# Kernel optimization log

Hardware: AMD Instinct MI355X
Metric: run time of the kernel (lower is better)

The kernel has to match this reference:

```python
import jax, jax.numpy as jnp
import numpy as np

N = 2048

def setup_inputs() -> dict:
    key = jax.random.key(0)
    k0, k1, k2, k3 = jax.random.split(key, 4)
    return {
        "input": jax.random.normal(k0, (N, N), dtype=jnp.float32),
        "weight1": jax.random.normal(k1, (N, N), dtype=jnp.float32),
        "weight2": jax.random.normal(k2, (N, N), dtype=jnp.float32),
        "weight3": jax.random.normal(k3, (N, N), dtype=jnp.float32),
    }

def reference(input, weight1, weight2, weight3):
    # Faithful translation of the torch DAG (duplicate mm kept: t4 == t2,
    # so t8 is mathematically zero, but we preserve the original math).
    t1 = input @ weight1
    t2 = input @ weight2
    t3 = weight3 @ weight3
    t4 = input @ weight2
    t5 = t1 * weight1
    t6 = (t5 @ input) * weight1
    t7 = t1 * t2 + t1 + t3
    t8 = t2 - t4
    t9 = t7 * t8 + t6 * t3
    t11 = t3 * t9
    t12 = t3 * (t1 @ input) * t6
    t13 = t7 + t11
    t14 = t8 + t12
    t15 = t13 + t14
    return t15
```

## Files before the change

### kernel.cpp

```cpp
#include <hip/hip_runtime.h>
#include <hip/hip_bf16.h>
#include <stdint.h>

#define NN 2048
#define BK 32

typedef __bf16 bf16;
typedef __bf16 bf16x8 __attribute__((ext_vector_type(8)));
typedef __bf16 bf16x4 __attribute__((ext_vector_type(4)));
typedef float f32x4 __attribute__((ext_vector_type(4)));

__device__ __forceinline__ void async_copy16(bf16* lds, const bf16* g) {
    __builtin_amdgcn_global_load_lds(
        (const __attribute__((address_space(1))) unsigned int*)g,
        (__attribute__((address_space(3))) unsigned int*)lds,
        16, 0, 0);
}

#define WAIT_VM(n) asm volatile("s_waitcnt vmcnt(" #n ")" ::: "memory")
#define BAR()                                  \
    do {                                       \
        asm volatile("" ::: "memory");         \
        __builtin_amdgcn_s_barrier();          \
        asm volatile("" ::: "memory");         \
    } while (0)

struct CastArgs {
    const float* in[4];
    bf16*        outT[4];
    bf16*        outN[4];
};

__global__ __launch_bounds__(256) void transpose_cast_kernel(CastArgs args) {
    const float* __restrict__ in = args.in[blockIdx.z];
    bf16* __restrict__ outT      = args.outT[blockIdx.z];
    bf16* __restrict__ outN      = args.outN[blockIdx.z];
    __shared__ float tile[64][65];
    const int bx = blockIdx.x * 64;
    const int by = blockIdx.y * 64;
    const int t  = threadIdx.x;
    const int c4 = (t & 15) * 4, r0 = t >> 4;
#pragma unroll
    for (int p = 0; p < 4; ++p) {
        const int r = r0 + p * 16;
        const float4 v = *(const float4*)&in[(size_t)(by + r) * NN + bx + c4];
        tile[r][c4 + 0] = v.x; tile[r][c4 + 1] = v.y;
        tile[r][c4 + 2] = v.z; tile[r][c4 + 3] = v.w;
        if (outN) {
            bf16x4 b = {(bf16)v.x, (bf16)v.y, (bf16)v.z, (bf16)v.w};
            *(bf16x4*)&outN[(size_t)(by + r) * NN + bx + c4] = b;
        }
    }
    __syncthreads();
    const int cc8 = (t & 7) * 8, rw0 = t >> 3;
#pragma unroll
    for (int p = 0; p < 2; ++p) {
        const int rw = rw0 + p * 32;
        bf16x8 b;
#pragma unroll
        for (int i = 0; i < 8; ++i) b[i] = (bf16)tile[cc8 + i][rw];
        *(bf16x8*)&outT[(size_t)(bx + rw) * NN + by + cc8] = b;
    }
}

struct P1Args {
    const bf16*  Abf;
    const bf16*  W1t;
    const bf16*  W2t;
    const bf16*  W3bf;
    const bf16*  W3t;
    float*       M1;
    float*       M2out;
    float*       M3;
    const float* W1;
    bf16*        M1bf;
    bf16*        B1bf;
};

__global__ __launch_bounds__(256, 2) void phase1_kernel(P1Args a) {
    __shared__ bf16 As0[128 * BK], As1[128 * BK];
    __shared__ bf16 B10[128 * BK], B11[128 * BK];
    __shared__ bf16 B20[128 * BK], B21[128 * BK];

    const int t  = threadIdx.x;
    const int bm = blockIdx.x * 128;
    const int bn = blockIdx.y * 128;

    const int row0 = t >> 2;
    const int qp   = t & 3;
    const int col0 = ((qp ^ ((row0 >> 1) & 3)) << 3);
    const int off0 = t * 8;

    const int wave = t >> 6;
    const int lane = t & 63;
    const int wm   = (wave >> 1) * 64;
    const int wn   = (wave & 1) * 64;
    const int lrow = lane & 15;
    const int q    = lane >> 4;
    const int qe   = (q ^ ((lrow >> 1) & 3)) << 3;

    if (blockIdx.z == 0) {
        const bf16* gA  = a.Abf + (size_t)(bm + row0) * NN + col0;
        const bf16* gB1 = a.W1t + (size_t)(bn + row0) * NN + col0;
        const bf16* gB2 = a.W2t + (size_t)(bn + row0) * NN + col0;

        f32x4 acc1[4][4], acc2[4][4];
#pragma unroll
        for (int i = 0; i < 4; ++i)
#pragma unroll
            for (int j = 0; j < 4; ++j) {
                acc1[i][j] = (f32x4){0.f, 0.f, 0.f, 0.f};
                acc2[i][j] = (f32x4){0.f, 0.f, 0.f, 0.f};
            }

        auto issue = [&](bf16* As, bf16* B1, bf16* B2, int kt) {
            const int kof = kt * BK;
            async_copy16(&As[off0],           gA  + kof);
            async_copy16(&As[off0 + 64 * BK], gA  + (size_t)64 * NN + kof);
            async_copy16(&B1[off0],           gB1 + kof);
            async_copy16(&B1[off0 + 64 * BK], gB1 + (size_t)64 * NN + kof);
            async_copy16(&B2[off0],           gB2 + kof);
            async_copy16(&B2[off0 + 64 * BK], gB2 + (size_t)64 * NN + kof);
        };
        auto compute = [&](const bf16* As, const bf16* B1, const bf16* B2) {
            bf16x8 af[4], b1[4], b2[4];
#pragma unroll
            for (int i = 0; i < 4; ++i)
                af[i] = *(const bf16x8*)&As[(wm + i * 16 + lrow) * BK + qe];
#pragma unroll
            for (int j = 0; j < 4; ++j) {
                b1[j] = *(const bf16x8*)&B1[(wn + j * 16 + lrow) * BK + qe];
                b2[j] = *(const bf16x8*)&B2[(wn + j * 16 + lrow) * BK + qe];
            }
#pragma unroll
            for (int i = 0; i < 4; ++i)
#pragma unroll
                for (int j = 0; j < 4; ++j) {
                    acc1[i][j] = __builtin_amdgcn_mfma_f32_16x16x32_bf16(
                        af[i], b1[j], acc1[i][j], 0, 0, 0);
                    acc2[i][j] = __builtin_amdgcn_mfma_f32_16x16x32_bf16(
                        af[i], b2[j], acc2[i][j], 0, 0, 0);
                }
        };

        issue(As0, B10, B20, 0);
#pragma unroll 1
        for (int kt = 0; kt < 62; kt += 2) {
            issue(As1, B11, B21, kt + 1); WAIT_VM(6); BAR();
            compute(As0, B10, B20); BAR();
            issue(As0, B10, B20, kt + 2); WAIT_VM(6); BAR();
            compute(As1, B11, B21); BAR();
        }
        issue(As1, B11, B21, 63); WAIT_VM(6); BAR();
        compute(As0, B10, B20); BAR();
        WAIT_VM(0); BAR();
        compute(As1, B11, B21);

#pragma unroll
        for (int i = 0; i < 4; ++i)
#pragma unroll
            for (int j = 0; j < 4; ++j)
#pragma unroll
                for (int r = 0; r < 4; ++r) {
                    const size_t idx =
                        (size_t)(bm + wm + i * 16 + q * 4 + r) * NN +
                        (bn + wn + j * 16 + lrow);
                    const float v1 = acc1[i][j][r];
                    a.M1[idx]    = v1;
                    a.M2out[idx] = acc2[i][j][r];
                    const float w = a.W1[idx];
                    a.M1bf[idx] = (bf16)v1;
                    a.B1bf[idx] = (bf16)(v1 * w);
                }
    } else {
        const bf16* gA = a.W3bf + (size_t)(bm + row0) * NN + col0;
        const bf16* gB = a.W3t  + (size_t)(bn + row0) * NN + col0;

        f32x4 acc[4][4];
#pragma unroll
        for (int i = 0; i < 4; ++i)
#pragma unroll
            for (int j = 0; j < 4; ++j) acc[i][j] = (f32x4){0.f, 0.f, 0.f, 0.f};

        auto issue = [&](bf16* As, bf16* Bs, int kt) {
            const int kof = kt * BK;
            async_copy16(&As[off0],           gA + kof);
            async_copy16(&As[off0 + 64 * BK], gA + (size_t)64 * NN + kof);
            async_copy16(&Bs[off0],           gB + kof);
            async_copy16(&Bs[off0 + 64 * BK], gB + (size_t)64 * NN + kof);
        };
        auto compute = [&](const bf16* As, const bf16* Bs) {
            bf16x8 af[4], bfr[4];
#pragma unroll
            for (int i = 0; i < 4; ++i)
                af[i] = *(const bf16x8*)&As[(wm + i * 16 + lrow) * BK + qe];
#pragma unroll
            for (int j = 0; j < 4; ++j)
                bfr[j] = *(const bf16x8*)&Bs[(wn + j * 16 + lrow) * BK + qe];
#pragma unroll
            for (int i = 0; i < 4; ++i)
#pragma unroll
                for (int j = 0; j < 4; ++j)
                    acc[i][j] = __builtin_amdgcn_mfma_f32_16x16x32_bf16(
                        af[i], bfr[j], acc[i][j], 0, 0, 0);
        };

        issue(As0, B10, 0);
#pragma unroll 1
        for (int kt = 0; kt < 62; kt += 2) {
            issue(As1, B11, kt + 1); WAIT_VM(4); BAR();
            compute(As0, B10); BAR();
            issue(As0, B10, kt + 2); WAIT_VM(4); BAR();
            compute(As1, B11); BAR();
        }
        issue(As1, B11, 63); WAIT_VM(4); BAR();
        compute(As0, B10); BAR();
        WAIT_VM(0); BAR();
        compute(As1, B11);

#pragma unroll
        for (int i = 0; i < 4; ++i)
#pragma unroll
            for (int j = 0; j < 4; ++j)
#pragma unroll
                for (int r = 0; r < 4; ++r)
                    a.M3[(size_t)(bm + wm + i * 16 + q * 4 + r) * NN +
                         (bn + wn + j * 16 + lrow)] = acc[i][j][r];
    }
}

struct Gemm2Args {
    const bf16*  M1bf;
    const bf16*  B1bf;
    const bf16*  At;
    const float* M1;
    const float* M3;
    const float* W1;
    float*       out;
};

__global__ __launch_bounds__(256, 2) void gemm2_fused_kernel(Gemm2Args args) {
    __shared__ bf16 A50[128 * BK], A51[128 * BK], A52[128 * BK];
    __shared__ bf16 A40[128 * BK], A41[128 * BK], A42[128 * BK];
    __shared__ bf16 Bs0[64 * BK],  Bs1[64 * BK],  Bs2[64 * BK];

    const int t  = threadIdx.x;
    const int bm = blockIdx.x * 128;
    const int bn = blockIdx.y * 64;

    const int row0 = t >> 2;
    const int qp   = t & 3;
    const int col0 = ((qp ^ ((row0 >> 1) & 3)) << 3);
    const int off0 = t * 8;

    const bf16* g5 = args.M1bf + (size_t)(bm + row0) * NN + col0;
    const bf16* g4 = args.B1bf + (size_t)(bm + row0) * NN + col0;
    const bf16* gB = args.At   + (size_t)(bn + row0) * NN + col0;

    const int wave = t >> 6;
    const int lane = t & 63;
    const int wm   = wave * 32;
    const int lrow = lane & 15;
    const int q    = lane >> 4;
    const int qe   = (q ^ ((lrow >> 1) & 3)) << 3;

    f32x4 acc5[2][4], acc4[2][4];
#pragma unroll
    for (int i = 0; i < 2; ++i)
#pragma unroll
        for (int j = 0; j < 4; ++j) {
            acc5[i][j] = (f32x4){0.f, 0.f, 0.f, 0.f};
            acc4[i][j] = (f32x4){0.f, 0.f, 0.f, 0.f};
        }

    auto issue = [&](bf16* A5, bf16* A4, bf16* Bs, int kt) {
        const int kof = kt * BK;
        async_copy16(&A5[off0],           g5 + kof);
        async_copy16(&A5[off0 + 64 * BK], g5 + (size_t)64 * NN + kof);
        async_copy16(&A4[off0],           g4 + kof);
        async_copy16(&A4[off0 + 64 * BK], g4 + (size_t)64 * NN + kof);
        async_copy16(&Bs[off0],           gB + kof);
    };
    auto compute = [&](const bf16* A5, const bf16* A4, const bf16* Bs) {
        bf16x8 a5[2], a4[2], bfr[4];
#pragma unroll
        for (int i = 0; i < 2; ++i) {
            a5[i] = *(const bf16x8*)&A5[(wm + i * 16 + lrow) * BK + qe];
            a4[i] = *(const bf16x8*)&A4[(wm + i * 16 + lrow) * BK + qe];
        }
#pragma unroll
        for (int j = 0; j < 4; ++j)
            bfr[j] = *(const bf16x8*)&Bs[(j * 16 + lrow) * BK + qe];
#pragma unroll
        for (int i = 0; i < 2; ++i)
#pragma unroll
            for (int j = 0; j < 4; ++j) {
                acc5[i][j] = __builtin_amdgcn_mfma_f32_16x16x32_bf16(
                    a5[i], bfr[j], acc5[i][j], 0, 0, 0);
                acc4[i][j] = __builtin_amdgcn_mfma_f32_16x16x32_bf16(
                    a4[i], bfr[j], acc4[i][j], 0, 0, 0);
            }
    };

    issue(A50, A40, Bs0, 0);
    issue(A51, A41, Bs1, 1);
#pragma unroll 1
    for (int kt = 0; kt < 60; kt += 3) {
        issue(A52, A42, Bs2, kt + 2); WAIT_VM(10); BAR(); compute(A50, A40, Bs0); BAR();
        issue(A50, A40, Bs0, kt + 3); WAIT_VM(10); BAR(); compute(A51, A41, Bs1); BAR();
        issue(A51, A41, Bs1, kt + 4); WAIT_VM(10); BAR(); compute(A52, A42, Bs2); BAR();
    }
    issue(A52, A42, Bs2, 62); WAIT_VM(10); BAR(); compute(A50, A40, Bs0); BAR();
    issue(A50, A40, Bs0, 63); WAIT_VM(10); BAR(); compute(A51, A41, Bs1); BAR();
    WAIT_VM(5); BAR(); compute(A52, A42, Bs2); BAR();
    WAIT_VM(0); BAR(); compute(A50, A40, Bs0);

#pragma unroll
    for (int i = 0; i < 2; ++i)
#pragma unroll
        for (int j = 0; j < 4; ++j)
#pragma unroll
            for (int r = 0; r < 4; ++r) {
                const size_t idx = (size_t)(bm + wm + i * 16 + q * 4 + r) * NN +
                                   (bn + j * 16 + lrow);
                const float m5 = acc5[i][j][r];
                const float m4 = acc4[i][j][r];
                const float m1 = args.M1[idx];
                const float m3 = args.M3[idx];
                const float w1 = args.W1[idx];
                const float m2 = args.out[idx];
                args.out[idx] =
                    m1 * m2 + m1 + m3 + m3 * (m4 * w1) * (m3 + m5);
            }
}

extern "C" void kernel_launch(void* const* d_in, const int* in_sizes, int n_in,
                              void* d_out, int out_size, void* d_ws, size_t ws_size,
                              hipStream_t stream) {
    const float* A  = (const float*)d_in[0];
    const float* W1 = (const float*)d_in[1];
    const float* W2 = (const float*)d_in[2];
    const float* W3 = (const float*)d_in[3];
    float* out = (float*)d_out;

    const size_t P = (size_t)NN * NN;
    char* ws = (char*)d_ws;

    bf16* Abf  = (bf16*)ws;
    bf16* At   = Abf + P;
    bf16* W1t  = At + P;
    bf16* W2t  = W1t + P;
    bf16* W3bf = W2t + P;
    bf16* W3t  = W3bf + P;
    bf16* M1bf = W3t + P;
    bf16* B1bf = M1bf + P;
    float* M1  = (float*)(B1bf + P);
    float* M3  = M1 + P;

    CastArgs ca;
    ca.in[0] = A;  ca.outT[0] = At;  ca.outN[0] = Abf;
    ca.in[1] = W1; ca.outT[1] = W1t; ca.outN[1] = nullptr;
    ca.in[2] = W2; ca.outT[2] = W2t; ca.outN[2] = nullptr;
    ca.in[3] = W3; ca.outT[3] = W3t; ca.outN[3] = W3bf;
    transpose_cast_kernel<<<dim3(NN / 64, NN / 64, 4), 256, 0, stream>>>(ca);

    P1Args p1;
    p1.Abf = Abf; p1.W1t = W1t; p1.W2t = W2t; p1.W3bf = W3bf; p1.W3t = W3t;
    p1.M1 = M1; p1.M2out = out; p1.M3 = M3;
    p1.W1 = W1; p1.M1bf = M1bf; p1.B1bf = B1bf;
    phase1_kernel<<<dim3(NN / 128, NN / 128, 2), 256, 0, stream>>>(p1);

    Gemm2Args g2;
    g2.M1bf = M1bf; g2.B1bf = B1bf; g2.At = At;
    g2.M1 = M1; g2.M3 = M3; g2.W1 = W1; g2.out = out;
    gemm2_fused_kernel<<<dim3(NN / 128, NN / 64), 256, 0, stream>>>(g2);
}
```

Measured before the change: 232.7 us.

## Restructure GEMM kernels to 512 threads with 4-stage LDS pipeline and tile swizzle

Both GEMM kernels move to 512-thread blocks (8 waves) with a 4-buffer LDS ring that prefetches three K-tiles ahead, one barrier pair per K step, and s_setprio around the MFMA block. Block indices are swizzled into groups for L2 locality. The second GEMM's output tile widens from 128x64 to 128x128. The aim is to hide global-load latency and raise MFMA occupancy, at the cost of larger LDS use (about 96KB per block) that may cap residency at one block per CU.

```diff
diff --git a/kernel.cpp b/kernel.cpp
--- a/kernel.cpp
+++ b/kernel.cpp
@@ -4,6 +4,7 @@
 
 #define NN 2048
 #define BK 32
+#define NK (NN / BK)
 
 typedef __bf16 bf16;
 typedef __bf16 bf16x8 __attribute__((ext_vector_type(8)));
@@ -18,6 +19,7 @@
 }
 
 #define WAIT_VM(n) asm volatile("s_waitcnt vmcnt(" #n ")" ::: "memory")
+#define LGKM0()    asm volatile("s_waitcnt lgkmcnt(0)" ::: "memory")
 #define BAR()                                  \
     do {                                       \
         asm volatile("" ::: "memory");         \
@@ -77,89 +79,95 @@
     bf16*        B1bf;
 };
 
-__global__ __launch_bounds__(256, 2) void phase1_kernel(P1Args a) {
-    __shared__ bf16 As0[128 * BK], As1[128 * BK];
-    __shared__ bf16 B10[128 * BK], B11[128 * BK];
-    __shared__ bf16 B20[128 * BK], B21[128 * BK];
-
-    const int t  = threadIdx.x;
-    const int bm = blockIdx.x * 128;
-    const int bn = blockIdx.y * 128;
-
-    const int row0 = t >> 2;
-    const int qp   = t & 3;
-    const int col0 = ((qp ^ ((row0 >> 1) & 3)) << 3);
+__global__ __launch_bounds__(512, 2) void gemm_dual_kernel(P1Args a) {
+    __shared__ __align__(16) bf16 LA[4][128 * BK];
+    __shared__ __align__(16) bf16 LB[4][128 * BK];
+    __shared__ __align__(16) bf16 LC[4][128 * BK];
+
+    const int t = threadIdx.x;
+    const int wg  = blockIdx.y * 16 + blockIdx.x;
+    const int swz = (wg & 7) * 32 + (wg >> 3);
+    const int bm  = (swz >> 4) * 128;
+    const int bn  = (swz & 15) * 128;
+
+    const int srow = t >> 2;
+    const int sch  = t & 3;
+    const int scol = ((sch ^ ((srow >> 1) & 3)) << 3);
     const int off0 = t * 8;
 
     const int wave = t >> 6;
     const int lane = t & 63;
-    const int wm   = (wave >> 1) * 64;
-    const int wn   = (wave & 1) * 64;
     const int lrow = lane & 15;
     const int q    = lane >> 4;
     const int qe   = (q ^ ((lrow >> 1) & 3)) << 3;
 
     if (blockIdx.z == 0) {
-        const bf16* gA  = a.Abf + (size_t)(bm + row0) * NN + col0;
-        const bf16* gB1 = a.W1t + (size_t)(bn + row0) * NN + col0;
-        const bf16* gB2 = a.W2t + (size_t)(bn + row0) * NN + col0;
-
-        f32x4 acc1[4][4], acc2[4][4];
+        const int wm = (wave >> 2) * 64;
+        const int wn = (wave & 3) * 32;
+
+        const bf16* gA  = a.Abf + (size_t)(bm + srow) * NN + scol;
+        const bf16* gB1 = a.W1t + (size_t)(bn + srow) * NN + scol;
+        const bf16* gB2 = a.W2t + (size_t)(bn + srow) * NN + scol;
+
+        f32x4 acc1[4][2], acc2[4][2];
 #pragma unroll
         for (int i = 0; i < 4; ++i)
 #pragma unroll
-            for (int j = 0; j < 4; ++j) {
+            for (int j = 0; j < 2; ++j) {
                 acc1[i][j] = (f32x4){0.f, 0.f, 0.f, 0.f};
                 acc2[i][j] = (f32x4){0.f, 0.f, 0.f, 0.f};
             }
 
-        auto issue = [&](bf16* As, bf16* B1, bf16* B2, int kt) {
+        auto issue = [&](int buf, int kt) {
             const int kof = kt * BK;
-            async_copy16(&As[off0],           gA  + kof);
-            async_copy16(&As[off0 + 64 * BK], gA  + (size_t)64 * NN + kof);
-            async_copy16(&B1[off0],           gB1 + kof);
-            async_copy16(&B1[off0 + 64 * BK], gB1 + (size_t)64 * NN + kof);
-            async_copy16(&B2[off0],           gB2 + kof);
-            async_copy16(&B2[off0 + 64 * BK], gB2 + (size_t)64 * NN + kof);
+            async_copy16(&LA[buf][off0], gA  + kof);
+            async_copy16(&LB[buf][off0], gB1 + kof);
+            async_copy16(&LC[buf][off0], gB2 + kof);
         };
-        auto compute = [&](const bf16* As, const bf16* B1, const bf16* B2) {
-            bf16x8 af[4], b1[4], b2[4];
+
+        issue(0, 0); issue(1, 1); issue(2, 2);
+        WAIT_VM(6); BAR();
+
+#pragma unroll 1
+        for (int kt = 0; kt < NK; ++kt) {
+            const int b = kt & 3;
+            const bf16* cA = LA[b];
+            const bf16* cB = LB[b];
+            const bf16* cC = LC[b];
+
+            bf16x8 af[4], f1[2], f2[2];
 #pragma unroll
             for (int i = 0; i < 4; ++i)
-                af[i] = *(const bf16x8*)&As[(wm + i * 16 + lrow) * BK + qe];
-#pragma unroll
-            for (int j = 0; j < 4; ++j) {
-                b1[j] = *(const bf16x8*)&B1[(wn + j * 16 + lrow) * BK + qe];
-                b2[j] = *(const bf16x8*)&B2[(wn + j * 16 + lrow) * BK + qe];
+                af[i] = *(const bf16x8*)&cA[(wm + i * 16 + lrow) * BK + qe];
+#pragma unroll
+            for (int j = 0; j < 2; ++j) {
+                f1[j] = *(const bf16x8*)&cB[(wn + j * 16 + lrow) * BK + qe];
+                f2[j] = *(const bf16x8*)&cC[(wn + j * 16 + lrow) * BK + qe];
             }
+            if (kt < NK - 3) issue((kt + 3) & 3, kt + 3);
+
+            BAR(); LGKM0();
+            __builtin_amdgcn_s_setprio(1);
 #pragma unroll
             for (int i = 0; i < 4; ++i)
 #pragma unroll
-                for (int j = 0; j < 4; ++j) {
+                for (int j = 0; j < 2; ++j) {
                     acc1[i][j] = __builtin_amdgcn_mfma_f32_16x16x32_bf16(
-                        af[i], b1[j], acc1[i][j], 0, 0, 0);
+                        af[i], f1[j], acc1[i][j], 0, 0, 0);
                     acc2[i][j] = __builtin_amdgcn_mfma_f32_16x16x32_bf16(
-                        af[i], b2[j], acc2[i][j], 0, 0, 0);
+                        af[i], f2[j], acc2[i][j], 0, 0, 0);
                 }
-        };
-
-        issue(As0, B10, B20, 0);
-#pragma unroll 1
-        for (int kt = 0; kt < 62; kt += 2) {
-            issue(As1, B11, B21, kt + 1); WAIT_VM(6); BAR();
-            compute(As0, B10, B20); BAR();
-            issue(As0, B10, B20, kt + 2); WAIT_VM(6); BAR();
-            compute(As1, B11, B21); BAR();
-        }
-        issue(As1, B11, B21, 63); WAIT_VM(6); BAR();
-        compute(As0, B10, B20); BAR();
-        WAIT_VM(0); BAR();
-        compute(As1, B11, B21);
+            __builtin_amdgcn_s_setprio(0);
+            if (kt < NK - 3)       { WAIT_VM(6); }
+            else if (kt == NK - 3) { WAIT_VM(3); }
+            else                   { WAIT_VM(0); }
+            BAR();
+        }
 
 #pragma unroll
         for (int i = 0; i < 4; ++i)
 #pragma unroll
-            for (int j = 0; j < 4; ++j)
+            for (int j = 0; j < 2; ++j)
 #pragma unroll
                 for (int r = 0; r < 4; ++r) {
                     const size_t idx =
@@ -173,55 +181,61 @@
                     a.B1bf[idx] = (bf16)(v1 * w);
                 }
     } else {
-        const bf16* gA = a.W3bf + (size_t)(bm + row0) * NN + col0;
-        const bf16* gB = a.W3t  + (size_t)(bn + row0) * NN + col0;
-
-        f32x4 acc[4][4];
+        const int wm = (wave >> 2) * 64;
+        const int wn = (wave & 3) * 32;
+
+        const bf16* gA = a.W3bf + (size_t)(bm + srow) * NN + scol;
+        const bf16* gB = a.W3t  + (size_t)(bn + srow) * NN + scol;
+
+        f32x4 acc[4][2];
 #pragma unroll
         for (int i = 0; i < 4; ++i)
 #pragma unroll
-            for (int j = 0; j < 4; ++j) acc[i][j] = (f32x4){0.f, 0.f, 0.f, 0.f};
-
-        auto issue = [&](bf16* As, bf16* Bs, int kt) {
+            for (int j = 0; j < 2; ++j) acc[i][j] = (f32x4){0.f, 0.f, 0.f, 0.f};
+
+        auto issue = [&](int buf, int kt) {
             const int kof = kt * BK;
-            async_copy16(&As[off0],           gA + kof);
-            async_copy16(&As[off0 + 64 * BK], gA + (size_t)64 * NN + kof);
-            async_copy16(&Bs[off0],           gB + kof);
-            async_copy16(&Bs[off0 + 64 * BK], gB + (size_t)64 * NN + kof);
+            async_copy16(&LA[buf][off0], gA + kof);
+            async_copy16(&LB[buf][off0], gB + kof);
         };
-        auto compute = [&](const bf16* As, const bf16* Bs) {
-            bf16x8 af[4], bfr[4];
+
+        issue(0, 0); issue(1, 1); issue(2, 2);
+        WAIT_VM(4); BAR();
+
+#pragma unroll 1
+        for (int kt = 0; kt < NK; ++kt) {
+            const int b = kt & 3;
+            const bf16* cA = LA[b];
+            const bf16* cB = LB[b];
+
+            bf16x8 af[4], f1[2];
 #pragma unroll
             for (int i = 0; i < 4; ++i)
-                af[i] = *(const bf16x8*)&As[(wm + i * 16 + lrow) * BK + qe];
-#pragma unroll
-            for (int j = 0; j < 4; ++j)
-                bfr[j] = *(const bf16x8*)&Bs[(wn + j * 16 + lrow) * BK + qe];
+                af[i] = *(const bf16x8*)&cA[(wm + i * 16 + lrow) * BK + qe];
+#pragma unroll
+            for (int j = 0; j < 2; ++j)
+                f1[j] = *(const bf16x8*)&cB[(wn + j * 16 + lrow) * BK + qe];
+            if (kt < NK - 3) issue((kt + 3) & 3, kt + 3);
+
+            BAR(); LGKM0();
+            __builtin_amdgcn_s_setprio(1);
 #pragma unroll
             for (int i = 0; i < 4; ++i)
 #pragma unroll
-                for (int j = 0; j < 4; ++j)
+                for (int j = 0; j < 2; ++j)
                     acc[i][j] = __builtin_amdgcn_mfma_f32_16x16x32_bf16(
-                        af[i], bfr[j], acc[i][j], 0, 0, 0);
-        };
-
-        issue(As0, B10, 0);
-#pragma unroll 1
-        for (int kt = 0; kt < 62; kt += 2) {
-            issue(As1, B11, kt + 1); WAIT_VM(4); BAR();
-            compute(As0, B10); BAR();
-            issue(As0, B10, kt + 2); WAIT_VM(4); BAR();
-            compute(As1, B11); BAR();
-        }
-        issue(As1, B11, 63); WAIT_VM(4); BAR();
-        compute(As0, B10); BAR();
-        WAIT_VM(0); BAR();
-        compute(As1, B11);
+                        af[i], f1[j], acc[i][j], 0, 0, 0);
+            __builtin_amdgcn_s_setprio(0);
+            if (kt < NK - 3)       { WAIT_VM(4); }
+            else if (kt == NK - 3) { WAIT_VM(2); }
+            else                   { WAIT_VM(0); }
+            BAR();
+        }
 
 #pragma unroll
         for (int i = 0; i < 4; ++i)
 #pragma unroll
-            for (int j = 0; j < 4; ++j)
+            for (int j = 0; j < 2; ++j)
 #pragma unroll
                 for (int r = 0; r < 4; ++r)
                     a.M3[(size_t)(bm + wm + i * 16 + q * 4 + r) * NN +
@@ -239,31 +253,34 @@
     float*       out;
 };
 
-__global__ __launch_bounds__(256, 2) void gemm2_fused_kernel(Gemm2Args args) {
-    __shared__ bf16 A50[128 * BK], A51[128 * BK], A52[128 * BK];
-    __shared__ bf16 A40[128 * BK], A41[128 * BK], A42[128 * BK];
-    __shared__ bf16 Bs0[64 * BK],  Bs1[64 * BK],  Bs2[64 * BK];
-
-    const int t  = threadIdx.x;
-    const int bm = blockIdx.x * 128;
-    const int bn = blockIdx.y * 64;
-
-    const int row0 = t >> 2;
-    const int qp   = t & 3;
-    const int col0 = ((qp ^ ((row0 >> 1) & 3)) << 3);
+__global__ __launch_bounds__(512, 2) void gemm2_fused_kernel(Gemm2Args a) {
+    __shared__ __align__(16) bf16 L5[4][128 * BK];
+    __shared__ __align__(16) bf16 L4[4][128 * BK];
+    __shared__ __align__(16) bf16 LBt[4][128 * BK];
+
+    const int t = threadIdx.x;
+    const int wg  = blockIdx.y * 16 + blockIdx.x;
+    const int swz = (wg & 7) * 32 + (wg >> 3);
+    const int bm  = (swz >> 4) * 128;
+    const int bn  = (swz & 15) * 128;
+
+    const int srow = t >> 2;
+    const int sch  = t & 3;
+    const int scol = ((sch ^ ((srow >> 1) & 3)) << 3);
     const int off0 = t * 8;
-
-    const bf16* g5 = args.M1bf + (size_t)(bm + row0) * NN + col0;
-    const bf16* g4 = args.B1bf + (size_t)(bm + row0) * NN + col0;
-    const bf16* gB = args.At   + (size_t)(bn + row0) * NN + col0;
 
     const int wave = t >> 6;
     const int lane = t & 63;
-    const int wm   = wave * 32;
+    const int wm   = (wave >> 1) * 32;
+    const int wn   = (wave & 1) * 64;
     const int lrow = lane & 15;
     const int q    = lane >> 4;
     const int qe   = (q ^ ((lrow >> 1) & 3)) << 3;
 
+    const bf16* g5 = a.M1bf + (size_t)(bm + srow) * NN + scol;
+    const bf16* g4 = a.B1bf + (size_t)(bm + srow) * NN + scol;
+    const bf16* gB = a.At   + (size_t)(bn + srow) * NN + scol;
+
     f32x4 acc5[2][4], acc4[2][4];
 #pragma unroll
     for (int i = 0; i < 2; ++i)
@@ -273,24 +290,36 @@
             acc4[i][j] = (f32x4){0.f, 0.f, 0.f, 0.f};
         }
 
-    auto issue = [&](bf16* A5, bf16* A4, bf16* Bs, int kt) {
+    auto issue = [&](int buf, int kt) {
         const int kof = kt * BK;
-        async_copy16(&A5[off0],           g5 + kof);
-        async_copy16(&A5[off0 + 64 * BK], g5 + (size_t)64 * NN + kof);
-        async_copy16(&A4[off0],           g4 + kof);
-        async_copy16(&A4[off0 + 64 * BK], g4 + (size_t)64 * NN + kof);
-        async_copy16(&Bs[off0],           gB + kof);
+        async_copy16(&L5[buf][off0],  g5 + kof);
+        async_copy16(&L4[buf][off0],  g4 + kof);
+        async_copy16(&LBt[buf][off0], gB + kof);
     };
-    auto compute = [&](const bf16* A5, const bf16* A4, const bf16* Bs) {
+
+    issue(0, 0); issue(1, 1); issue(2, 2);
+    WAIT_VM(6); BAR();
+
+#pragma unroll 1
+    for (int kt = 0; kt < NK; ++kt) {
+        const int b = kt & 3;
+        const bf16* c5 = L5[b];
+        const bf16* c4 = L4[b];
+        const bf16* cB = LBt[b];
+
         bf16x8 a5[2], a4[2], bfr[4];
 #pragma unroll
         for (int i = 0; i < 2; ++i) {
-            a5[i] = *(const bf16x8*)&A5[(wm + i * 16 + lrow) * BK + qe];
-            a4[i] = *(const bf16x8*)&A4[(wm + i * 16 + lrow) * BK + qe];
+            a5[i] = *(const bf16x8*)&c5[(wm + i * 16 + lrow) * BK + qe];
+            a4[i] = *(const bf16x8*)&c4[(wm + i * 16 + lrow) * BK + qe];
         }
 #pragma unroll
         for (int j = 0; j < 4; ++j)
-            bfr[j] = *(const bf16x8*)&Bs[(j * 16 + lrow) * BK + qe];
+            bfr[j] = *(const bf16x8*)&cB[(wn + j * 16 + lrow) * BK + qe];
+        if (kt < NK - 3) issue((kt + 3) & 3, kt + 3);
+
+        BAR(); LGKM0();
+        __builtin_amdgcn_s_setprio(1);
 #pragma unroll
         for (int i = 0; i < 2; ++i)
 #pragma unroll
@@ -300,20 +329,12 @@
                 acc4[i][j] = __builtin_amdgcn_mfma_f32_16x16x32_bf16(
                     a4[i], bfr[j], acc4[i][j], 0, 0, 0);
             }
-    };
-
-    issue(A50, A40, Bs0, 0);
-    issue(A51, A41, Bs1, 1);
-#pragma unroll 1
-    for (int kt = 0; kt < 60; kt += 3) {
-        issue(A52, A42, Bs2, kt + 2); WAIT_VM(10); BAR(); compute(A50, A40, Bs0); BAR();
-        issue(A50, A40, Bs0, kt + 3); WAIT_VM(10); BAR(); compute(A51, A41, Bs1); BAR();
-        issue(A51, A41, Bs1, kt + 4); WAIT_VM(10); BAR(); compute(A52, A42, Bs2); BAR();
+        __builtin_amdgcn_s_setprio(0);
+        if (kt < NK - 3)       { WAIT_VM(6); }
+        else if (kt == NK - 3) { WAIT_VM(3); }
+        else                   { WAIT_VM(0); }
+        BAR();
     }
-    issue(A52, A42, Bs2, 62); WAIT_VM(10); BAR(); compute(A50, A40, Bs0); BAR();
-    issue(A50, A40, Bs0, 63); WAIT_VM(10); BAR(); compute(A51, A41, Bs1); BAR();
-    WAIT_VM(5); BAR(); compute(A52, A42, Bs2); BAR();
-    WAIT_VM(0); BAR(); compute(A50, A40, Bs0);
 
 #pragma unroll
     for (int i = 0; i < 2; ++i)
@@ -322,15 +343,14 @@
 #pragma unroll
             for (int r = 0; r < 4; ++r) {
                 const size_t idx = (size_t)(bm + wm + i * 16 + q * 4 + r) * NN +
-                                   (bn + j * 16 + lrow);
+                                   (bn + wn + j * 16 + lrow);
                 const float m5 = acc5[i][j][r];
                 const float m4 = acc4[i][j][r];
-                const float m1 = args.M1[idx];
-                const float m3 = args.M3[idx];
-                const float w1 = args.W1[idx];
-                const float m2 = args.out[idx];
-                args.out[idx] =
-                    m1 * m2 + m1 + m3 + m3 * (m4 * w1) * (m3 + m5);
+                const float m1 = a.M1[idx];
+                const float m3 = a.M3[idx];
+                const float w1 = a.W1[idx];
+                const float m2 = a.out[idx];
+                a.out[idx] = m1 * m2 + m1 + m3 + m3 * (m4 * w1) * (m3 + m5);
             }
 }
 
@@ -368,10 +388,10 @@
     p1.Abf = Abf; p1.W1t = W1t; p1.W2t = W2t; p1.W3bf = W3bf; p1.W3t = W3t;
     p1.M1 = M1; p1.M2out = out; p1.M3 = M3;
     p1.W1 = W1; p1.M1bf = M1bf; p1.B1bf = B1bf;
-    phase1_kernel<<<dim3(NN / 128, NN / 128, 2), 256, 0, stream>>>(p1);
+    gemm_dual_kernel<<<dim3(NN / 128, NN / 128, 2), 512, 0, stream>>>(p1);
 
     Gemm2Args g2;
     g2.M1bf = M1bf; g2.B1bf = B1bf; g2.At = At;
     g2.M1 = M1; g2.M3 = M3; g2.W1 = W1; g2.out = out;
-    gemm2_fused_kernel<<<dim3(NN / 128, NN / 64), 256, 0, stream>>>(g2);
-}
+    gemm2_fused_kernel<<<dim3(NN / 128, NN / 128), 512, 0, stream>>>(g2);
+}
```

Measured after the change: 237.2 us. No clear change (+1.9%).

## Triple-buffer phase1 GEMM LDS tiles to prefetch two k-steps ahead

Applied to the files above, without the earlier changes.

Replaces the double-buffered LDS pipeline in phase1 with a three-stage ring buffer, issuing async global-to-LDS loads two tiles ahead of the compute step. The goal is to hide more global memory latency behind the MFMA work. In exchange, LDS use per block rises by half, which could limit occupancy. The loop also becomes a single-step loop with modulo buffer indexing.

```diff
diff --git a/kernel.cpp b/kernel.cpp
--- a/kernel.cpp
+++ b/kernel.cpp
@@ -4,6 +4,7 @@
 
 #define NN 2048
 #define BK 32
+#define NK (NN / BK)
 
 typedef __bf16 bf16;
 typedef __bf16 bf16x8 __attribute__((ext_vector_type(8)));
@@ -78,9 +79,9 @@
 };
 
 __global__ __launch_bounds__(256, 2) void phase1_kernel(P1Args a) {
-    __shared__ bf16 As0[128 * BK], As1[128 * BK];
-    __shared__ bf16 B10[128 * BK], B11[128 * BK];
-    __shared__ bf16 B20[128 * BK], B21[128 * BK];
+    __shared__ __align__(16) bf16 LA[3][128 * BK];
+    __shared__ __align__(16) bf16 LB[3][128 * BK];
+    __shared__ __align__(16) bf16 LC[3][128 * BK];
 
     const int t  = threadIdx.x;
     const int bm = blockIdx.x * 128;
@@ -113,14 +114,14 @@
                 acc2[i][j] = (f32x4){0.f, 0.f, 0.f, 0.f};
             }
 
-        auto issue = [&](bf16* As, bf16* B1, bf16* B2, int kt) {
+        auto issue = [&](int buf, int kt) {
             const int kof = kt * BK;
-            async_copy16(&As[off0],           gA  + kof);
-            async_copy16(&As[off0 + 64 * BK], gA  + (size_t)64 * NN + kof);
-            async_copy16(&B1[off0],           gB1 + kof);
-            async_copy16(&B1[off0 + 64 * BK], gB1 + (size_t)64 * NN + kof);
-            async_copy16(&B2[off0],           gB2 + kof);
-            async_copy16(&B2[off0 + 64 * BK], gB2 + (size_t)64 * NN + kof);
+            async_copy16(&LA[buf][off0],           gA  + kof);
+            async_copy16(&LA[buf][off0 + 64 * BK], gA  + (size_t)64 * NN + kof);
+            async_copy16(&LB[buf][off0],           gB1 + kof);
+            async_copy16(&LB[buf][off0 + 64 * BK], gB1 + (size_t)64 * NN + kof);
+            async_copy16(&LC[buf][off0],           gB2 + kof);
+            async_copy16(&LC[buf][off0 + 64 * BK], gB2 + (size_t)64 * NN + kof);
         };
         auto compute = [&](const bf16* As, const bf16* B1, const bf16* B2) {
             bf16x8 af[4], b1[4], b2[4];
@@ -143,18 +144,17 @@
                 }
         };
 
-        issue(As0, B10, B20, 0);
+        issue(0, 0); issue(1, 1);
 #pragma unroll 1
-        for (int kt = 0; kt < 62; kt += 2) {
-            issue(As1, B11, B21, kt + 1); WAIT_VM(6); BAR();
-            compute(As0, B10, B20); BAR();
-            issue(As0, B10, B20, kt + 2); WAIT_VM(6); BAR();
-            compute(As1, B11, B21); BAR();
-        }
-        issue(As1, B11, B21, 63); WAIT_VM(6); BAR();
-        compute(As0, B10, B20); BAR();
-        WAIT_VM(0); BAR();
-        compute(As1, B11, B21);
+        for (int kt = 0; kt < NK; ++kt) {
+            if (kt < NK - 2)       { issue((kt + 2) % 3, kt + 2); WAIT_VM(12); }
+            else if (kt == NK - 2) { WAIT_VM(6); }
+            else                   { WAIT_VM(0); }
+            BAR();
+            const int b = kt % 3;
+            compute(LA[b], LB[b], LC[b]);
+            BAR();
+        }
 
 #pragma unroll
         for (int i = 0; i < 4; ++i)
@@ -182,12 +182,12 @@
 #pragma unroll
             for (int j = 0; j < 4; ++j) acc[i][j] = (f32x4){0.f, 0.f, 0.f, 0.f};
 
-        auto issue = [&](bf16* As, bf16* Bs, int kt) {
+        auto issue = [&](int buf, int kt) {
             const int kof = kt * BK;
-            async_copy16(&As[off0],           gA + kof);
-            async_copy16(&As[off0 + 64 * BK], gA + (size_t)64 * NN + kof);
-            async_copy16(&Bs[off0],           gB + kof);
-            async_copy16(&Bs[off0 + 64 * BK], gB + (size_t)64 * NN + kof);
+            async_copy16(&LA[buf][off0],           gA + kof);
+            async_copy16(&LA[buf][off0 + 64 * BK], gA + (size_t)64 * NN + kof);
+            async_copy16(&LB[buf][off0],           gB + kof);
+            async_copy16(&LB[buf][off0 + 64 * BK], gB + (size_t)64 * NN + kof);
         };
         auto compute = [&](const bf16* As, const bf16* Bs) {
             bf16x8 af[4], bfr[4];
@@ -205,18 +205,17 @@
                         af[i], bfr[j], acc[i][j], 0, 0, 0);
         };
 
-        issue(As0, B10, 0);
+        issue(0, 0); issue(1, 1);
 #pragma unroll 1
-        for (int kt = 0; kt < 62; kt += 2) {
-            issue(As1, B11, kt + 1); WAIT_VM(4); BAR();
-            compute(As0, B10); BAR();
-            issue(As0, B10, kt + 2); WAIT_VM(4); BAR();
-            compute(As1, B11); BAR();
-        }
-        issue(As1, B11, 63); WAIT_VM(4); BAR();
-        compute(As0, B10); BAR();
-        WAIT_VM(0); BAR();
-        compute(As1, B11);
+        for (int kt = 0; kt < NK; ++kt) {
+            if (kt < NK - 2)       { issue((kt + 2) % 3, kt + 2); WAIT_VM(8); }
+            else if (kt == NK - 2) { WAIT_VM(4); }
+            else                   { WAIT_VM(0); }
+            BAR();
+            const int b = kt % 3;
+            compute(LA[b], LB[b]);
+            BAR();
+        }
 
 #pragma unroll
         for (int i = 0; i < 4; ++i)
```

Result: slower. 240.6 us (+3.4%).

## Merge cast, phase1 and gemm2 into one cooperative persistent kernel

Applied to the files above, without the earlier changes.

Replaces the three kernel launches with a single cooperative kernel of 512 workgroups that runs the transpose-cast, the first GEMM phase and the fused second GEMM in sequence, separated by grid-wide syncs. Each workgroup handles 8 cast tiles in a loop and one tile of each GEMM phase, with shared memory carved out of one 60KB buffer. The aim is to remove launch gaps and kernel-boundary drains. In exchange it adds grid-sync cost, forces a fixed 512-block grid with 2 blocks per CU, and falls back to three separate launches if the cooperative launch fails.

```diff
diff --git a/kernel.cpp b/kernel.cpp
--- a/kernel.cpp
+++ b/kernel.cpp
@@ -1,6 +1,9 @@
 #include <hip/hip_runtime.h>
 #include <hip/hip_bf16.h>
+#include <hip/hip_cooperative_groups.h>
 #include <stdint.h>
+
+namespace cg = cooperative_groups;
 
 #define NN 2048
 #define BK 32
@@ -25,45 +28,10 @@
         asm volatile("" ::: "memory");         \
     } while (0)
 
-struct CastArgs {
-    const float* in[4];
-    bf16*        outT[4];
-    bf16*        outN[4];
-};
-
-__global__ __launch_bounds__(256) void transpose_cast_kernel(CastArgs args) {
-    const float* __restrict__ in = args.in[blockIdx.z];
-    bf16* __restrict__ outT      = args.outT[blockIdx.z];
-    bf16* __restrict__ outN      = args.outN[blockIdx.z];
-    __shared__ float tile[64][65];
-    const int bx = blockIdx.x * 64;
-    const int by = blockIdx.y * 64;
-    const int t  = threadIdx.x;
-    const int c4 = (t & 15) * 4, r0 = t >> 4;
-#pragma unroll
-    for (int p = 0; p < 4; ++p) {
-        const int r = r0 + p * 16;
-        const float4 v = *(const float4*)&in[(size_t)(by + r) * NN + bx + c4];
-        tile[r][c4 + 0] = v.x; tile[r][c4 + 1] = v.y;
-        tile[r][c4 + 2] = v.z; tile[r][c4 + 3] = v.w;
-        if (outN) {
-            bf16x4 b = {(bf16)v.x, (bf16)v.y, (bf16)v.z, (bf16)v.w};
-            *(bf16x4*)&outN[(size_t)(by + r) * NN + bx + c4] = b;
-        }
-    }
-    __syncthreads();
-    const int cc8 = (t & 7) * 8, rw0 = t >> 3;
-#pragma unroll
-    for (int p = 0; p < 2; ++p) {
-        const int rw = rw0 + p * 32;
-        bf16x8 b;
-#pragma unroll
-        for (int i = 0; i < 8; ++i) b[i] = (bf16)tile[cc8 + i][rw];
-        *(bf16x8*)&outT[(size_t)(bx + rw) * NN + by + cc8] = b;
-    }
-}
-
-struct P1Args {
+struct MegaArgs {
+    const float* cin[4];
+    bf16*        coutT[4];
+    bf16*        coutN[4];
     const bf16*  Abf;
     const bf16*  W1t;
     const bf16*  W2t;
@@ -75,16 +43,59 @@
     const float* W1;
     bf16*        M1bf;
     bf16*        B1bf;
+    const bf16*  At;
+    float*       out;
 };
 
-__global__ __launch_bounds__(256, 2) void phase1_kernel(P1Args a) {
-    __shared__ bf16 As0[128 * BK], As1[128 * BK];
-    __shared__ bf16 B10[128 * BK], B11[128 * BK];
-    __shared__ bf16 B20[128 * BK], B21[128 * BK];
+__device__ __forceinline__ void cast_phase(const MegaArgs& a, char* smemraw,
+                                           int unit) {
+    float* tile = (float*)smemraw;
+    const int z   = unit >> 10;
+    const int rem = unit & 1023;
+    const int bx  = (rem & 31) * 64;
+    const int by  = (rem >> 5) * 64;
+    const float* __restrict__ in = a.cin[z];
+    bf16* __restrict__ outT      = a.coutT[z];
+    bf16* __restrict__ outN      = a.coutN[z];
 
     const int t  = threadIdx.x;
-    const int bm = blockIdx.x * 128;
-    const int bn = blockIdx.y * 128;
+    const int c4 = (t & 15) * 4, r0 = t >> 4;
+#pragma unroll
+    for (int p = 0; p < 4; ++p) {
+        const int r = r0 + p * 16;
+        const float4 v = *(const float4*)&in[(size_t)(by + r) * NN + bx + c4];
+        tile[r * 65 + c4 + 0] = v.x; tile[r * 65 + c4 + 1] = v.y;
+        tile[r * 65 + c4 + 2] = v.z; tile[r * 65 + c4 + 3] = v.w;
+        if (outN) {
+            bf16x4 b = {(bf16)v.x, (bf16)v.y, (bf16)v.z, (bf16)v.w};
+            *(bf16x4*)&outN[(size_t)(by + r) * NN + bx + c4] = b;
+        }
+    }
+    __syncthreads();
+    const int cc8 = (t & 7) * 8, rw0 = t >> 3;
+#pragma unroll
+    for (int p = 0; p < 2; ++p) {
+        const int rw = rw0 + p * 32;
+        bf16x8 b;
+#pragma unroll
+        for (int i = 0; i < 8; ++i) b[i] = (bf16)tile[(cc8 + i) * 65 + rw];
+        *(bf16x8*)&outT[(size_t)(bx + rw) * NN + by + cc8] = b;
+    }
+}
+
+__device__ __forceinline__ void phase1_phase(const MegaArgs& a, char* smemraw,
+                                             int wg) {
+    bf16* As0 = (bf16*)smemraw;
+    bf16* As1 = As0 + 4096;
+    bf16* B10 = As0 + 2 * 4096;
+    bf16* B11 = As0 + 3 * 4096;
+    bf16* B20 = As0 + 4 * 4096;
+    bf16* B21 = As0 + 5 * 4096;
+
+    const int t  = threadIdx.x;
+    const int bm = (wg & 15) * 128;
+    const int bn = ((wg >> 4) & 15) * 128;
+    const int z  = wg >> 8;
 
     const int row0 = t >> 2;
     const int qp   = t & 3;
@@ -99,7 +110,7 @@
     const int q    = lane >> 4;
     const int qe   = (q ^ ((lrow >> 1) & 3)) << 3;
 
-    if (blockIdx.z == 0) {
+    if (z == 0) {
         const bf16* gA  = a.Abf + (size_t)(bm + row0) * NN + col0;
         const bf16* gB1 = a.W1t + (size_t)(bn + row0) * NN + col0;
         const bf16* gB2 = a.W2t + (size_t)(bn + row0) * NN + col0;
@@ -229,33 +240,30 @@
     }
 }
 
-struct Gemm2Args {
-    const bf16*  M1bf;
-    const bf16*  B1bf;
-    const bf16*  At;
-    const float* M1;
-    const float* M3;
-    const float* W1;
-    float*       out;
-};
-
-__global__ __launch_bounds__(256, 2) void gemm2_fused_kernel(Gemm2Args args) {
-    __shared__ bf16 A50[128 * BK], A51[128 * BK], A52[128 * BK];
-    __shared__ bf16 A40[128 * BK], A41[128 * BK], A42[128 * BK];
-    __shared__ bf16 Bs0[64 * BK],  Bs1[64 * BK],  Bs2[64 * BK];
+__device__ __forceinline__ void gemm2_phase(const MegaArgs& a, char* smemraw,
+                                            int wg) {
+    bf16* A50 = (bf16*)smemraw;
+    bf16* A51 = A50 + 4096;
+    bf16* A52 = A50 + 2 * 4096;
+    bf16* A40 = A50 + 3 * 4096;
+    bf16* A41 = A50 + 4 * 4096;
+    bf16* A42 = A50 + 5 * 4096;
+    bf16* Bs0 = A50 + 6 * 4096;
+    bf16* Bs1 = Bs0 + 2048;
+    bf16* Bs2 = Bs0 + 2 * 2048;
 
     const int t  = threadIdx.x;
-    const int bm = blockIdx.x * 128;
-    const int bn = blockIdx.y * 64;
+    const int bm = (wg & 15) * 128;
+    const int bn = (wg >> 4) * 64;
 
     const int row0 = t >> 2;
     const int qp   = t & 3;
     const int col0 = ((qp ^ ((row0 >> 1) & 3)) << 3);
     const int off0 = t * 8;
 
-    const bf16* g5 = args.M1bf + (size_t)(bm + row0) * NN + col0;
-    const bf16* g4 = args.B1bf + (size_t)(bm + row0) * NN + col0;
-    const bf16* gB = args.At   + (size_t)(bn + row0) * NN + col0;
+    const bf16* g5 = a.M1bf + (size_t)(bm + row0) * NN + col0;
+    const bf16* g4 = a.B1bf + (size_t)(bm + row0) * NN + col0;
+    const bf16* gB = a.At   + (size_t)(bn + row0) * NN + col0;
 
     const int wave = t >> 6;
     const int lane = t & 63;
@@ -325,13 +333,48 @@
                                    (bn + j * 16 + lrow);
                 const float m5 = acc5[i][j][r];
                 const float m4 = acc4[i][j][r];
-                const float m1 = args.M1[idx];
-                const float m3 = args.M3[idx];
-                const float w1 = args.W1[idx];
-                const float m2 = args.out[idx];
-                args.out[idx] =
-                    m1 * m2 + m1 + m3 + m3 * (m4 * w1) * (m3 + m5);
+                const float m1 = a.M1[idx];
+                const float m3 = a.M3[idx];
+                const float w1 = a.W1[idx];
+                const float m2 = a.out[idx];
+                a.out[idx] = m1 * m2 + m1 + m3 + m3 * (m4 * w1) * (m3 + m5);
             }
+}
+
+__global__ __launch_bounds__(256, 2) void mega_kernel(MegaArgs a) {
+    __shared__ __align__(16) char smem[61440];
+    const int wg = blockIdx.x;
+
+#pragma unroll 1
+    for (int u = 0; u < 8; ++u) {
+        __syncthreads();
+        cast_phase(a, smem, wg * 8 + u);
+    }
+    __threadfence();
+    cg::this_grid().sync();
+
+    phase1_phase(a, smem, wg);
+    __threadfence();
+    cg::this_grid().sync();
+
+    gemm2_phase(a, smem, wg);
+}
+
+__global__ __launch_bounds__(256) void cast_sa(MegaArgs a) {
+    __shared__ __align__(16) char smem[64 * 65 * 4];
+#pragma unroll 1
+    for (int u = 0; u < 8; ++u) {
+        __syncthreads();
+        cast_phase(a, smem, blockIdx.x * 8 + u);
+    }
+}
+__global__ __launch_bounds__(256, 2) void phase1_sa(MegaArgs a) {
+    __shared__ __align__(16) char smem[6 * 4096 * 2];
+    phase1_phase(a, smem, blockIdx.x);
+}
+__global__ __launch_bounds__(256, 2) void gemm2_sa(MegaArgs a) {
+    __shared__ __align__(16) char smem[61440];
+    gemm2_phase(a, smem, blockIdx.x);
 }
 
 extern "C" void kernel_launch(void* const* d_in, const int* in_sizes, int n_in,
@@ -357,21 +400,23 @@
     float* M1  = (float*)(B1bf + P);
     float* M3  = M1 + P;
 
-    CastArgs ca;
-    ca.in[0] = A;  ca.outT[0] = At;  ca.outN[0] = Abf;
-    ca.in[1] = W1; ca.outT[1] = W1t; ca.outN[1] = nullptr;
-    ca.in[2] = W2; ca.outT[2] = W2t; ca.outN[2] = nullptr;
-    ca.in[3] = W3; ca.outT[3] = W3t; ca.outN[3] = W3bf;
-    transpose_cast_kernel<<<dim3(NN / 64, NN / 64, 4), 256, 0, stream>>>(ca);
-
-    P1Args p1;
-    p1.Abf = Abf; p1.W1t = W1t; p1.W2t = W2t; p1.W3bf = W3bf; p1.W3t = W3t;
-    p1.M1 = M1; p1.M2out = out; p1.M3 = M3;
-    p1.W1 = W1; p1.M1bf = M1bf; p1.B1bf = B1bf;
-    phase1_kernel<<<dim3(NN / 128, NN / 128, 2), 256, 0, stream>>>(p1);
-
-    Gemm2Args g2;
-    g2.M1bf = M1bf; g2.B1bf = B1bf; g2.At = At;
-    g2.M1 = M1; g2.M3 = M3; g2.W1 = W1; g2.out = out;
-    gemm2_fused_kernel<<<dim3(NN / 128, NN / 64), 256, 0, stream>>>(g2);
-}
+    MegaArgs ma;
+    ma.cin[0] = A;  ma.coutT[0] = At;  ma.coutN[0] = Abf;
+    ma.cin[1] = W1; ma.coutT[1] = W1t; ma.coutN[1] = nullptr;
+    ma.cin[2] = W2; ma.coutT[2] = W2t; ma.coutN[2] = nullptr;
+    ma.cin[3] = W3; ma.coutT[3] = W3t; ma.coutN[3] = W3bf;
+    ma.Abf = Abf; ma.W1t = W1t; ma.W2t = W2t; ma.W3bf = W3bf; ma.W3t = W3t;
+    ma.M1 = M1; ma.M2out = out; ma.M3 = M3;
+    ma.W1 = W1; ma.M1bf = M1bf; ma.B1bf = B1bf;
+    ma.At = At; ma.out = out;
+
+    void* params[] = {(void*)&ma};
+    hipError_t err = hipLaunchCooperativeKernel(
+        (const void*)mega_kernel, dim3(512), dim3(256), params, 0, stream);
+    if (err != hipSuccess) {
+        (void)hipGetLastError();
+        cast_sa<<<dim3(512), 256, 0, stream>>>(ma);
+        phase1_sa<<<dim3(512), 256, 0, stream>>>(ma);
+        gemm2_sa<<<dim3(512), 256, 0, stream>>>(ma);
+    }
+}
```

Result: slower. 508.1 us (+118.3%).
